# Kernel tuning notes

Hardware: AMD Instinct MI355X
Metric: run time of the kernel (lower is better)

Reference implementation:

```python
import jax, jax.numpy as jnp
import numpy as np

B, S, H = 32, 2048, 1024
A = 1024  # attention_hidden_size
EPS = 1e-5


def setup_inputs() -> dict:
    key = jax.random.key(0)
    ks = jax.random.split(key, 16)
    sc_h = 1.0 / np.sqrt(H)
    sc_a = 1.0 / np.sqrt(A)
    sc_2h = 1.0 / np.sqrt(2 * H)
    return {
        "seq_states": jax.random.normal(ks[0], (B, S, H), jnp.float32),
        "q_state": jax.random.normal(ks[1], (B, H), jnp.float32),
        "Wk": jax.random.uniform(ks[2], (H, A), jnp.float32, -sc_h, sc_h),
        "bk": jax.random.uniform(ks[3], (A,), jnp.float32, -sc_h, sc_h),
        "Wq": jax.random.uniform(ks[4], (H, A), jnp.float32, -sc_h, sc_h),
        "bq": jax.random.uniform(ks[5], (A,), jnp.float32, -sc_h, sc_h),
        "Wg": jax.random.uniform(ks[6], (A, A), jnp.float32, -sc_a, sc_a),
        "bg": jax.random.uniform(ks[7], (A,), jnp.float32, -sc_a, sc_a),
        "Ws": jax.random.uniform(ks[8], (A, 1), jnp.float32, -sc_a, sc_a),
        "bs": jax.random.uniform(ks[9], (1,), jnp.float32, -sc_a, sc_a),
        "Wo": jax.random.uniform(ks[10], (2 * H, H), jnp.float32, -sc_2h, sc_2h),
        "bo": jax.random.uniform(ks[11], (H,), jnp.float32, -sc_2h, sc_2h),
        "gamma": jnp.ones((H,), jnp.float32),
        "beta": jnp.zeros((H,), jnp.float32),
    }


def reference(seq_states, q_state, Wk, bk, Wq, bq, Wg, bg, Ws, bs, Wo, bo, gamma, beta):
    keys = jnp.einsum("bsh,ha->bsa", seq_states, Wk) + bk          # [B,S,A]
    query = (q_state @ Wq + bq)[:, None, :]                          # [B,1,A]
    alignment = jnp.tanh(keys + query)                               # [B,S,A]
    gate = jax.nn.sigmoid(jnp.einsum("bsa,ac->bsc", alignment, Wg) + bg)
    gated = alignment * gate                                         # dropout p=0.0 -> identity
    scores = jnp.einsum("bsa,ao->bso", gated, Ws)[..., 0] + bs[0]    # [B,S]
    weights = jax.nn.softmax(scores, axis=1)                         # [B,S]
    context = jnp.einsum("bs,bsh->bh", weights, seq_states)          # [B,H]
    fused_in = jnp.concatenate([context, q_state], axis=-1)          # [B,2H]
    pre = fused_in @ Wo + bo + q_state                               # residual
    mu = jnp.mean(pre, axis=-1, keepdims=True)
    var = jnp.var(pre, axis=-1, keepdims=True)
    fused = (pre - mu) * jax.lax.rsqrt(var + EPS) * gamma + beta
    return (fused, weights)
```

## Files before the change

### kernel.cpp

```cpp
#include <hip/hip_runtime.h>

typedef __attribute__((ext_vector_type(8))) short bf16x8;
typedef __attribute__((ext_vector_type(8))) unsigned short ushort8;
typedef __attribute__((ext_vector_type(4))) unsigned short ushortx4;
typedef __attribute__((ext_vector_type(4))) float f32x4;

#define BM 256
#define BN 256
#define BK 64

__device__ __forceinline__ unsigned short f2bf(float f) {
  union { float f; unsigned u; } c; c.f = f;
  return (unsigned short)((c.u + 0x7fffu + ((c.u >> 16) & 1u)) >> 16);
}
__device__ __forceinline__ float bf2f(unsigned short u) {
  union { unsigned u; float f; } c; c.u = ((unsigned)u) << 16;
  return c.f;
}
__device__ __forceinline__ float fast_tanh(float x) {
  float e = __expf(2.f * x);
  return 1.f - 2.f * __builtin_amdgcn_rcpf(e + 1.f);
}
__device__ __forceinline__ float fast_sigmoid(float x) {
  return __builtin_amdgcn_rcpf(1.f + __expf(-x));
}
__device__ __forceinline__ void gload16(const void* g, void* lds) {
  __builtin_amdgcn_global_load_lds(
      (const __attribute__((address_space(1))) unsigned int*)g,
      (__attribute__((address_space(3))) unsigned int*)lds, 16, 0, 0);
}
__device__ __forceinline__ void bar() {
  asm volatile("" ::: "memory");
  __builtin_amdgcn_s_barrier();
  asm volatile("" ::: "memory");
}
__device__ __forceinline__ void lgkm0_fence() {
  asm volatile("s_waitcnt lgkmcnt(0)" ::: "memory");
  __builtin_amdgcn_sched_barrier(0);
}
template <int N> __device__ __forceinline__ void vwait() {
  if constexpr (N < 0) {
  } else if constexpr (N == 6) asm volatile("s_waitcnt vmcnt(6)" ::: "memory");
  else if constexpr (N == 0) asm volatile("s_waitcnt vmcnt(0)" ::: "memory");
}

__device__ __forceinline__ void mfma_q(const bf16x8 (&av)[2][4], const bf16x8 (&bv)[2][2],
                                       int qm, int qn, f32x4 (&acc)[8][4]) {
  __builtin_amdgcn_s_setprio(1);
#pragma unroll
  for (int kk = 0; kk < 2; ++kk)
#pragma unroll
    for (int i = 0; i < 4; ++i)
#pragma unroll
      for (int j = 0; j < 2; ++j)
        acc[qm * 4 + i][qn * 2 + j] = __builtin_amdgcn_mfma_f32_16x16x32_bf16(
            av[kk][i], bv[kk][j], acc[qm * 4 + i][qn * 2 + j], 0, 0, 0);
  __builtin_amdgcn_s_setprio(0);
}

template <bool S1, bool S234, int WEND>
__device__ __forceinline__ void ktile(
    const char* rA0, const char* rA1,
    const char* rB0, const char* rB1,
    char* dNxtA, char* dCurA, char* dCurB,
    const unsigned short* pA0, const unsigned short* pA1,
    const unsigned short* pB0, const unsigned short* pB1,
    int kA1, int k2, f32x4 (&acc)[8][4]) {
  bf16x8 av[2][4], a2[2][4], bv0[2][2], bv1[2][2];
#pragma unroll
  for (int kk = 0; kk < 2; ++kk) {
    const char* ra = kk ? rA1 : rA0;
    const char* rb = kk ? rB1 : rB0;
#pragma unroll
    for (int i = 0; i < 4; ++i) av[kk][i] = *(const bf16x8*)(ra + i * 2048);
#pragma unroll
    for (int j = 0; j < 2; ++j) bv0[kk][j] = *(const bf16x8*)(rb + j * 2048);
  }
  if (S1) {
    gload16(pA0 + 65536 + kA1, dNxtA + 16384);
    gload16(pA1 + 65536 + kA1, dNxtA + 16384 + 8192);
  }
  bar();
  lgkm0_fence();
  mfma_q(av, bv0, 0, 0, acc);
  bar();
#pragma unroll
  for (int kk = 0; kk < 2; ++kk) {
    const char* rb = kk ? rB1 : rB0;
#pragma unroll
    for (int j = 0; j < 2; ++j) bv1[kk][j] = *(const bf16x8*)(rb + 16384 + j * 2048);
  }
  if (S234) {
    gload16(pA0 + k2, dCurA);
    gload16(pA1 + k2, dCurA + 8192);
  }
  bar();
  lgkm0_fence();
  mfma_q(av, bv1, 0, 1, acc);
  bar();
#pragma unroll
  for (int kk = 0; kk < 2; ++kk) {
    const char* ra = kk ? rA1 : rA0;
#pragma unroll
    for (int i = 0; i < 4; ++i) a2[kk][i] = *(const bf16x8*)(ra + 16384 + i * 2048);
  }
  if (S234) {
    gload16(pB0 + k2, dCurB);
    gload16(pB1 + k2, dCurB + 8192);
  }
  bar();
  lgkm0_fence();
  mfma_q(a2, bv1, 1, 1, acc);
  bar();
  if (S234) {
    gload16(pB0 + 32768 + k2, dCurB + 16384);
    gload16(pB1 + 32768 + k2, dCurB + 16384 + 8192);
  }
  bar();
  mfma_q(a2, bv0, 1, 0, acc);
  vwait<WEND>();
  bar();
}

#define GEMM_SETUP_AND_PIPELINE(Ag, Bg)                                                    \
  int t = threadIdx.x, lane = t & 63, wave = t >> 6;                                       \
  int wr = wave >> 2, wc = wave & 3;                                                       \
  int sl0 = ((lane >> 4) ^ (lane & 7)) * 16;                                               \
  int sl1 = (((lane >> 4) + 4) ^ (lane & 7)) * 16;                                         \
  int aLane = (wr * 64 + (lane & 15)) * 128;                                               \
  int bLane = (wc * 32 + (lane & 15)) * 128;                                               \
  const char* rA0k0 = (const char*)As0 + aLane + sl0;                                      \
  const char* rA0k1 = (const char*)As0 + aLane + sl1;                                      \
  const char* rA1k0 = (const char*)As1 + aLane + sl0;                                      \
  const char* rA1k1 = (const char*)As1 + aLane + sl1;                                      \
  const char* rB0k0 = (const char*)Bs0 + bLane + sl0;                                      \
  const char* rB0k1 = (const char*)Bs0 + bLane + sl1;                                      \
  const char* rB1k0 = (const char*)Bs1 + bLane + sl0;                                      \
  const char* rB1k1 = (const char*)Bs1 + bLane + sl1;                                      \
  char* dA0 = (char*)As0 + t * 16;                                                         \
  char* dA1 = (char*)As1 + t * 16;                                                         \
  char* dB0 = (char*)Bs0 + t * 16;                                                         \
  char* dB1 = (char*)Bs1 + t * 16;                                                         \
  int l3 = t >> 3;                                                                         \
  int sgE = ((t & 7) ^ (l3 & 7)) * 8;                                                      \
  const unsigned short* pA0 = Ag + (size_t)(m0 + l3) * 1024 + sgE;                         \
  const unsigned short* pA1 = pA0 + (size_t)128 * 1024;                                    \
  int nB0 = ((l3 >> 5) << 6) + (l3 & 31);                                                  \
  const unsigned short* pB0 = Bg + (size_t)(n0 + nB0) * 1024 + sgE;                        \
  const unsigned short* pB1 = pB0 + (size_t)128 * 1024;                                    \
  f32x4 acc[8][4] = {};                                                                    \
                      \
  gload16(pA0, dA0); gload16(pA1, dA0 + 8192);                                             \
  gload16(pB0, dB0); gload16(pB1, dB0 + 8192);                                             \
  gload16(pB0 + 32768, dB0 + 16384); gload16(pB1 + 32768, dB0 + 16384 + 8192);             \
  gload16(pA0 + 65536, dA0 + 16384); gload16(pA1 + 65536, dA0 + 16384 + 8192);             \
  gload16(pA0 + 64, dA1); gload16(pA1 + 64, dA1 + 8192);                                   \
  gload16(pB0 + 64, dB1); gload16(pB1 + 64, dB1 + 8192);                                   \
  gload16(pB0 + 32768 + 64, dB1 + 16384); gload16(pB1 + 32768 + 64, dB1 + 16384 + 8192);   \
  vwait<6>();                                                                              \
  bar();                                                                                   \
  _Pragma("unroll 1") for (int kt = 0; kt < 14; kt += 2) {                                 \
    ktile<true, true, 6>(rA0k0, rA0k1, rB0k0, rB0k1, dA1, dA0, dB0, pA0, pA1, pB0, pB1,    \
                         (kt + 1) * 64, (kt + 2) * 64, acc);                               \
    ktile<true, true, 6>(rA1k0, rA1k1, rB1k0, rB1k1, dA0, dA1, dB1, pA0, pA1, pB0, pB1,    \
                         (kt + 2) * 64, (kt + 3) * 64, acc);                               \
  }                                                                                        \
  ktile<true, false, 0>(rA0k0, rA0k1, rB0k0, rB0k1, dA1, dA0, dB0, pA0, pA1, pB0, pB1,     \
                        15 * 64, 0, acc);                                                  \
  ktile<false, false, -1>(rA1k0, rA1k1, rB1k0, rB1k1, dA0, dA1, dB1, pA0, pA1, pB0, pB1,   \
                          0, 0, acc);

__device__ __forceinline__ void tile_coords(int bid, int& m0, int& n0, int& nt) {
  int lin = (bid & 7) * 128 + (bid >> 3);
  int mt = lin >> 2;
  nt = lin & 3;
  m0 = mt * BM;
  n0 = nt * BN;
}

__global__ __launch_bounds__(256) void prep_kernel(
    const float* __restrict__ seq, unsigned short* __restrict__ seqb,
    const float* __restrict__ Wk, const float* __restrict__ Wg,
    unsigned short* __restrict__ WkT, unsigned short* __restrict__ WgT,
    const float* __restrict__ q, const float* __restrict__ Wq,
    float* __restrict__ qp) {
  __shared__ float smem[4160];
  int bid = blockIdx.x, t = threadIdx.x;
  if (bid < 2048) {
    size_t i = ((size_t)bid * 256 + t) * 8;
    const size_t stride = (size_t)2048 * 256 * 8;
    for (; i < (size_t)67108864; i += stride) {
      f32x4 v0 = *(const f32x4*)(seq + i);
      f32x4 v1 = *(const f32x4*)(seq + i + 4);
      ushort8 o;
#pragma unroll
      for (int k = 0; k < 4; ++k) { o[k] = f2bf(v0[k]); o[k + 4] = f2bf(v1[k]); }
      *(ushort8*)(seqb + i) = o;
    }
  } else if (bid < 2560) {
    int b2 = bid - 2048;
    int mat = b2 >> 8;
    int tid = b2 & 255;
    int tr = tid >> 4, tc = tid & 15;
    const float* src = mat ? Wg : Wk;
    unsigned short* dst = mat ? WgT : WkT;
    int r0 = tr * 64, c0 = tc * 64;
    int lr = t >> 6, lc = t & 63;
#pragma unroll
    for (int i = 0; i < 16; ++i) {
      int r = i * 4 + lr;
      smem[r * 65 + lc] = src[(size_t)(r0 + r) * 1024 + c0 + lc];
    }
    __syncthreads();
#pragma unroll
    for (int i = 0; i < 16; ++i) {
      int r = i * 4 + lr;
      dst[(size_t)(c0 + r) * 1024 + r0 + lc] = f2bf(smem[lc * 65 + r]);
    }
  } else {
    int b3 = bid - 2560;
    int ac = b3 & 3, hc = b3 >> 2;
    int h0 = hc * 128;
    for (int i = t; i < 4096; i += 256) {
      int b = i >> 7, hh = i & 127;
      smem[b * 128 + hh] = q[(size_t)b * 1024 + h0 + hh];
    }
    __syncthreads();
    int a = ac * 256 + t;
    float acc[32] = {};
    for (int hh = 0; hh < 128; hh += 4) {
      float w0 = Wq[(size_t)(h0 + hh) * 1024 + a];
      float w1 = Wq[(size_t)(h0 + hh + 1) * 1024 + a];
      float w2 = Wq[(size_t)(h0 + hh + 2) * 1024 + a];
      float w3 = Wq[(size_t)(h0 + hh + 3) * 1024 + a];
#pragma unroll
      for (int b = 0; b < 32; ++b) {
        f32x4 qv = *(const f32x4*)&smem[b * 128 + hh];
        acc[b] += qv[0] * w0 + qv[1] * w1 + qv[2] * w2 + qv[3] * w3;
      }
    }
#pragma unroll
    for (int b = 0; b < 32; ++b) qp[((size_t)(hc * 32 + b)) * 1024 + a] = acc[b];
  }
}

__global__ __launch_bounds__(512, 2) void gemm1_kernel(
    const unsigned short* __restrict__ seqb, const unsigned short* __restrict__ WkT,
    const float* __restrict__ qp, const float* __restrict__ bq,
    const float* __restrict__ bk, unsigned short* __restrict__ alignb) {
  __shared__ unsigned short As0[BM * BK], Bs0[BN * BK], As1[BM * BK], Bs1[BN * BK];
  int m0, n0, nt;
  tile_coords(blockIdx.x, m0, n0, nt);
  GEMM_SETUP_AND_PIPELINE(seqb, WkT)

  int bidx = m0 >> 11;
  float qv[4];
#pragma unroll
  for (int ni = 0; ni < 4; ++ni) {
    int col = n0 + wc * 64 + ni * 16 + (lane & 15);
    float s = bq[col] + bk[col];
#pragma unroll
    for (int hc = 0; hc < 8; ++hc) s += qp[((size_t)(hc * 32 + bidx)) * 1024 + col];
    qv[ni] = s;
  }
#pragma unroll
  for (int mi = 0; mi < 8; ++mi) {
    int row0 = m0 + wr * 128 + mi * 16 + ((lane >> 4) * 4);
#pragma unroll
    for (int ni = 0; ni < 4; ++ni) {
      int col = n0 + wc * 64 + ni * 16 + (lane & 15);
#pragma unroll
      for (int j = 0; j < 4; ++j) {
        float v = fast_tanh(acc[mi][ni][j] + qv[ni]);
        alignb[(size_t)(row0 + j) * 1024 + col] = f2bf(v);
      }
    }
  }
}

__global__ __launch_bounds__(512, 2) void gemm2_kernel(
    const unsigned short* __restrict__ alignb, const unsigned short* __restrict__ WgT,
    const float* __restrict__ bg, const float* __restrict__ Ws,
    float* __restrict__ scores_part) {
  __shared__ unsigned short As0[BM * BK], Bs0[BN * BK], As1[BM * BK], Bs1[BN * BK];
  __shared__ float sred[BM * 4];
  int m0, n0, nt;
  tile_coords(blockIdx.x, m0, n0, nt);
  GEMM_SETUP_AND_PIPELINE(alignb, WgT)

#pragma unroll
  for (int mi = 0; mi < 8; ++mi) {
#pragma unroll
    for (int j = 0; j < 4; ++j) {
      int rloc = wr * 128 + mi * 16 + ((lane >> 4) * 4) + j;
      int row = m0 + rloc;
      float p = 0.f;
#pragma unroll
      for (int ni = 0; ni < 4; ++ni) {
        int col = n0 + wc * 64 + ni * 16 + (lane & 15);
        float gate = fast_sigmoid(acc[mi][ni][j] + bg[col]);
        float al = bf2f(alignb[(size_t)row * 1024 + col]);
        p += al * gate * Ws[col];
      }
      p += __shfl_xor(p, 1);
      p += __shfl_xor(p, 2);
      p += __shfl_xor(p, 4);
      p += __shfl_xor(p, 8);
      if ((lane & 15) == 0) sred[rloc * 4 + wc] = p;
    }
  }
  __syncthreads();
  if (t < 256)
    scores_part[(size_t)nt * 65536 + m0 + t] =
        sred[t * 4] + sred[t * 4 + 1] + sred[t * 4 + 2] + sred[t * 4 + 3];
}

__global__ __launch_bounds__(256) void softmax_kernel(const float* __restrict__ sp,
                                                      float* __restrict__ wout) {
  __shared__ float red[256];
  int b = blockIdx.x, t = threadIdx.x;
  float sc[8];
  float lmax = -1e30f;
#pragma unroll
  for (int i = 0; i < 8; ++i) {
    int s = i * 256 + t;
    float v = 0.f;
#pragma unroll
    for (int n = 0; n < 4; ++n) v += sp[(size_t)n * 65536 + b * 2048 + s];
    sc[i] = v;
    lmax = fmaxf(lmax, v);
  }
  red[t] = lmax;
  __syncthreads();
  for (int off = 128; off > 0; off >>= 1) {
    if (t < off) red[t] = fmaxf(red[t], red[t + off]);
    __syncthreads();
  }
  float mx = red[0];
  __syncthreads();
  float lsum = 0.f;
#pragma unroll
  for (int i = 0; i < 8; ++i) {
    sc[i] = expf(sc[i] - mx);
    lsum += sc[i];
  }
  red[t] = lsum;
  __syncthreads();
  for (int off = 128; off > 0; off >>= 1) {
    if (t < off) red[t] += red[t + off];
    __syncthreads();
  }
  float inv = 1.f / red[0];
#pragma unroll
  for (int i = 0; i < 8; ++i) wout[(size_t)b * 2048 + i * 256 + t] = sc[i] * inv;
}

__global__ __launch_bounds__(256) void context_kernel(const unsigned short* __restrict__ seqb,
                                                      const float* __restrict__ wts,
                                                      float* __restrict__ ctx_part) {
  __shared__ float wsh[256];
  int b = blockIdx.x, t = threadIdx.x, s0 = blockIdx.z * 256;
  int h0 = t * 4;
  wsh[t] = wts[(size_t)b * 2048 + s0 + t];
  __syncthreads();
  float a0 = 0.f, a1 = 0.f, a2 = 0.f, a3 = 0.f;
  const unsigned short* p = seqb + ((size_t)b * 2048 + s0) * 1024 + h0;
#pragma unroll 4
  for (int s = 0; s < 256; ++s) {
    ushortx4 v = *(const ushortx4*)(p + (size_t)s * 1024);
    float w = wsh[s];
    a0 += w * bf2f(v[0]);
    a1 += w * bf2f(v[1]);
    a2 += w * bf2f(v[2]);
    a3 += w * bf2f(v[3]);
  }
  float* dst = ctx_part + (size_t)(blockIdx.z * 32 + b) * 1024 + h0;
  dst[0] = a0; dst[1] = a1; dst[2] = a2; dst[3] = a3;
}

__global__ __launch_bounds__(256) void pre_kernel(const float* __restrict__ ctx_part,
                                                  const float* __restrict__ q,
                                                  const float* __restrict__ Wo,
                                                  float* __restrict__ pre_part) {
  __shared__ float fin[32 * 128];
  int kc = blockIdx.x, hc = blockIdx.y, t = threadIdx.x;
  int k0 = kc * 128, h0 = hc * 256;
  for (int i = t; i < 4096; i += 256) {
    int b = i >> 7, kk = i & 127, k = k0 + kk;
    float f;
    if (k < 1024) {
      f = 0.f;
#pragma unroll
      for (int s = 0; s < 8; ++s) f += ctx_part[((size_t)(s * 32 + b)) * 1024 + k];
    } else {
      f = q[(size_t)b * 1024 + (k - 1024)];
    }
    fin[b * 128 + kk] = f;
  }
  __syncthreads();
  int h = h0 + t;
  float acc[32] = {};
  for (int kk = 0; kk < 128; kk += 4) {
    float w0 = Wo[(size_t)(k0 + kk) * 1024 + h];
    float w1 = Wo[(size_t)(k0 + kk + 1) * 1024 + h];
    float w2 = Wo[(size_t)(k0 + kk + 2) * 1024 + h];
    float w3 = Wo[(size_t)(k0 + kk + 3) * 1024 + h];
#pragma unroll
    for (int b = 0; b < 32; ++b) {
      f32x4 fv = *(const f32x4*)&fin[b * 128 + kk];
      acc[b] += fv[0] * w0 + fv[1] * w1 + fv[2] * w2 + fv[3] * w3;
    }
  }
#pragma unroll
  for (int b = 0; b < 32; ++b) pre_part[((size_t)(kc * 32 + b)) * 1024 + h] = acc[b];
}

__global__ __launch_bounds__(256) void ln_kernel(const float* __restrict__ pre_part,
                                                 const float* __restrict__ q,
                                                 const float* __restrict__ bo,
                                                 const float* __restrict__ gamma,
                                                 const float* __restrict__ beta,
                                                 float* __restrict__ outF) {
  __shared__ float red[256];
  int b = blockIdx.x, t = threadIdx.x;
  float v[4];
  float lsum = 0.f;
#pragma unroll
  for (int i = 0; i < 4; ++i) {
    int h = i * 256 + t;
    float x = bo[h] + q[(size_t)b * 1024 + h];
#pragma unroll
    for (int kc = 0; kc < 16; ++kc) x += pre_part[((size_t)(kc * 32 + b)) * 1024 + h];
    v[i] = x;
    lsum += x;
  }
  red[t] = lsum;
  __syncthreads();
  for (int off = 128; off > 0; off >>= 1) {
    if (t < off) red[t] += red[t + off];
    __syncthreads();
  }
  float mu = red[0] * (1.f / 1024.f);
  __syncthreads();
  float lv = 0.f;
#pragma unroll
  for (int i = 0; i < 4; ++i) {
    float d = v[i] - mu;
    lv += d * d;
  }
  red[t] = lv;
  __syncthreads();
  for (int off = 128; off > 0; off >>= 1) {
    if (t < off) red[t] += red[t + off];
    __syncthreads();
  }
  float var = red[0] * (1.f / 1024.f);
  float rs = rsqrtf(var + 1e-5f);
#pragma unroll
  for (int i = 0; i < 4; ++i) {
    int h = i * 256 + t;
    outF[(size_t)b * 1024 + h] = (v[i] - mu) * rs * gamma[h] + beta[h];
  }
}

extern "C" void kernel_launch(void* const* d_in, const int* in_sizes, int n_in,
                              void* d_out, int out_size, void* d_ws, size_t ws_size,
                              hipStream_t stream) {
  const float* seq = (const float*)d_in[0];
  const float* q = (const float*)d_in[1];
  const float* Wk = (const float*)d_in[2];
  const float* bk = (const float*)d_in[3];
  const float* Wq = (const float*)d_in[4];
  const float* bq = (const float*)d_in[5];
  const float* Wg = (const float*)d_in[6];
  const float* bg = (const float*)d_in[7];
  const float* Ws = (const float*)d_in[8];
  const float* Wo = (const float*)d_in[10];
  const float* bo = (const float*)d_in[11];
  const float* gamma = (const float*)d_in[12];
  const float* beta = (const float*)d_in[13];

  float* outF = (float*)d_out;
  float* outW = outF + 32 * 1024;

  char* ws = (char*)d_ws;
  unsigned short* alignb = (unsigned short*)ws;  ws += (size_t)134217728;
  unsigned short* seqb = (unsigned short*)ws;    ws += (size_t)134217728;
  unsigned short* WkT = (unsigned short*)ws;     ws += 2097152;
  unsigned short* WgT = (unsigned short*)ws;     ws += 2097152;
  float* qp = (float*)ws;                        ws += 1048576;
  float* scores_part = (float*)ws;               ws += 1048576;
  float* ctx_part = (float*)ws;                  ws += 1048576;
  float* pre_part = (float*)ws;                  ws += 2097152;
  if (ws_size < (size_t)(ws - (char*)d_ws)) return;

  prep_kernel<<<2592, 256, 0, stream>>>(seq, seqb, Wk, Wg, WkT, WgT, q, Wq, qp);
  gemm1_kernel<<<1024, 512, 0, stream>>>(seqb, WkT, qp, bq, bk, alignb);
  gemm2_kernel<<<1024, 512, 0, stream>>>(alignb, WgT, bg, Ws, scores_part);
  softmax_kernel<<<32, 256, 0, stream>>>(scores_part, outW);
  context_kernel<<<dim3(32, 1, 8), 256, 0, stream>>>(seqb, outW, ctx_part);
  pre_kernel<<<dim3(16, 4), 256, 0, stream>>>(ctx_part, q, Wo, pre_part);
  ln_kernel<<<32, 256, 0, stream>>>(pre_part, q, bo, gamma, beta, outF);
}
```

Baseline: 501.8 us.

## Restructure GEMM k-tile pipeline to per-k-half MFMA blocks and split context wider

The GEMM inner k-tile is reorganised. Each phase now runs a full 4x4 MFMA block over one k-half (two phases per A row-half) instead of quadrant-by-quadrant across both k-halves. The prefetch schedule now loads only one tile ahead, with vmcnt(2) waits, rather than keeping two tiles in flight. This cuts register pressure and changes how global loads into LDS overlap with MFMA, at the risk of exposing more load latency. Separately, the context reduction is split into 16 sequence chunks instead of 8 for more parallelism, which adds more partial sums for pre_kernel to reduce.

```diff
diff --git a/kernel.cpp b/kernel.cpp
--- a/kernel.cpp
+++ b/kernel.cpp
@@ -40,85 +40,78 @@
 }
 template <int N> __device__ __forceinline__ void vwait() {
   if constexpr (N < 0) {
-  } else if constexpr (N == 6) asm volatile("s_waitcnt vmcnt(6)" ::: "memory");
+  } else if constexpr (N == 2) asm volatile("s_waitcnt vmcnt(2)" ::: "memory");
   else if constexpr (N == 0) asm volatile("s_waitcnt vmcnt(0)" ::: "memory");
 }
 
-__device__ __forceinline__ void mfma_q(const bf16x8 (&av)[2][4], const bf16x8 (&bv)[2][2],
-                                       int qm, int qn, f32x4 (&acc)[8][4]) {
+__device__ __forceinline__ void mfma16(const bf16x8 (&a)[4], const bf16x8 (&b)[4], int ro,
+                                       f32x4 (&acc)[8][4]) {
   __builtin_amdgcn_s_setprio(1);
 #pragma unroll
-  for (int kk = 0; kk < 2; ++kk)
-#pragma unroll
-    for (int i = 0; i < 4; ++i)
-#pragma unroll
-      for (int j = 0; j < 2; ++j)
-        acc[qm * 4 + i][qn * 2 + j] = __builtin_amdgcn_mfma_f32_16x16x32_bf16(
-            av[kk][i], bv[kk][j], acc[qm * 4 + i][qn * 2 + j], 0, 0, 0);
+  for (int i = 0; i < 4; ++i)
+#pragma unroll
+    for (int n = 0; n < 4; ++n)
+      acc[ro + i][n] =
+          __builtin_amdgcn_mfma_f32_16x16x32_bf16(a[i], b[n], acc[ro + i][n], 0, 0, 0);
   __builtin_amdgcn_s_setprio(0);
 }
 
-template <bool S1, bool S234, int WEND>
+template <bool ST, int W1, int W4>
 __device__ __forceinline__ void ktile(
-    const char* rA0, const char* rA1,
-    const char* rB0, const char* rB1,
-    char* dNxtA, char* dCurA, char* dCurB,
+    const char* rAk0, const char* rAk1,
+    const char* rBk0, const char* rBk1,
+    char* dNA, char* dNB,
     const unsigned short* pA0, const unsigned short* pA1,
     const unsigned short* pB0, const unsigned short* pB1,
-    int kA1, int k2, f32x4 (&acc)[8][4]) {
-  bf16x8 av[2][4], a2[2][4], bv0[2][2], bv1[2][2];
-#pragma unroll
-  for (int kk = 0; kk < 2; ++kk) {
-    const char* ra = kk ? rA1 : rA0;
-    const char* rb = kk ? rB1 : rB0;
-#pragma unroll
-    for (int i = 0; i < 4; ++i) av[kk][i] = *(const bf16x8*)(ra + i * 2048);
-#pragma unroll
-    for (int j = 0; j < 2; ++j) bv0[kk][j] = *(const bf16x8*)(rb + j * 2048);
-  }
-  if (S1) {
-    gload16(pA0 + 65536 + kA1, dNxtA + 16384);
-    gload16(pA1 + 65536 + kA1, dNxtA + 16384 + 8192);
-  }
+    int kN, f32x4 (&acc)[8][4]) {
+  bf16x8 a[4], a2[4], b[4];
+#pragma unroll
+  for (int i = 0; i < 4; ++i) a[i] = *(const bf16x8*)(rAk0 + i * 2048);
+#pragma unroll
+  for (int n = 0; n < 4; ++n)
+    b[n] = *(const bf16x8*)(rBk0 + (n >> 1) * 16384 + (n & 1) * 2048);
+  if (ST) {
+    gload16(pB0 + 32768 + kN, dNB + 16384);
+    gload16(pB1 + 32768 + kN, dNB + 16384 + 8192);
+  }
+  vwait<W1>();
   bar();
   lgkm0_fence();
-  mfma_q(av, bv0, 0, 0, acc);
-  bar();
-#pragma unroll
-  for (int kk = 0; kk < 2; ++kk) {
-    const char* rb = kk ? rB1 : rB0;
-#pragma unroll
-    for (int j = 0; j < 2; ++j) bv1[kk][j] = *(const bf16x8*)(rb + 16384 + j * 2048);
-  }
-  if (S234) {
-    gload16(pA0 + k2, dCurA);
-    gload16(pA1 + k2, dCurA + 8192);
+  mfma16(a, b, 0, acc);
+  bar();
+#pragma unroll
+  for (int i = 0; i < 4; ++i) a2[i] = *(const bf16x8*)(rAk0 + 16384 + i * 2048);
+  if (ST) {
+    gload16(pA0 + kN, dNA);
+    gload16(pA1 + kN, dNA + 8192);
   }
   bar();
   lgkm0_fence();
-  mfma_q(av, bv1, 0, 1, acc);
-  bar();
-#pragma unroll
-  for (int kk = 0; kk < 2; ++kk) {
-    const char* ra = kk ? rA1 : rA0;
-#pragma unroll
-    for (int i = 0; i < 4; ++i) a2[kk][i] = *(const bf16x8*)(ra + 16384 + i * 2048);
-  }
-  if (S234) {
-    gload16(pB0 + k2, dCurB);
-    gload16(pB1 + k2, dCurB + 8192);
+  mfma16(a2, b, 4, acc);
+  bar();
+#pragma unroll
+  for (int i = 0; i < 4; ++i) a[i] = *(const bf16x8*)(rAk1 + i * 2048);
+#pragma unroll
+  for (int n = 0; n < 4; ++n)
+    b[n] = *(const bf16x8*)(rBk1 + (n >> 1) * 16384 + (n & 1) * 2048);
+  if (ST) {
+    gload16(pB0 + kN, dNB);
+    gload16(pB1 + kN, dNB + 8192);
   }
   bar();
   lgkm0_fence();
-  mfma_q(a2, bv1, 1, 1, acc);
-  bar();
-  if (S234) {
-    gload16(pB0 + 32768 + k2, dCurB + 16384);
-    gload16(pB1 + 32768 + k2, dCurB + 16384 + 8192);
-  }
-  bar();
-  mfma_q(a2, bv0, 1, 0, acc);
-  vwait<WEND>();
+  mfma16(a, b, 0, acc);
+  bar();
+#pragma unroll
+  for (int i = 0; i < 4; ++i) a2[i] = *(const bf16x8*)(rAk1 + 16384 + i * 2048);
+  if (ST) {
+    gload16(pA0 + 65536 + kN, dNA + 16384);
+    gload16(pA1 + 65536 + kN, dNA + 16384 + 8192);
+  }
+  vwait<W4>();
+  bar();
+  lgkm0_fence();
+  mfma16(a2, b, 4, acc);
   bar();
 }
 
@@ -149,26 +142,21 @@
   const unsigned short* pB0 = Bg + (size_t)(n0 + nB0) * 1024 + sgE;                        \
   const unsigned short* pB1 = pB0 + (size_t)128 * 1024;                                    \
   f32x4 acc[8][4] = {};                                                                    \
-                      \
+             \
   gload16(pA0, dA0); gload16(pA1, dA0 + 8192);                                             \
   gload16(pB0, dB0); gload16(pB1, dB0 + 8192);                                             \
   gload16(pB0 + 32768, dB0 + 16384); gload16(pB1 + 32768, dB0 + 16384 + 8192);             \
   gload16(pA0 + 65536, dA0 + 16384); gload16(pA1 + 65536, dA0 + 16384 + 8192);             \
-  gload16(pA0 + 64, dA1); gload16(pA1 + 64, dA1 + 8192);                                   \
-  gload16(pB0 + 64, dB1); gload16(pB1 + 64, dB1 + 8192);                                   \
-  gload16(pB0 + 32768 + 64, dB1 + 16384); gload16(pB1 + 32768 + 64, dB1 + 16384 + 8192);   \
-  vwait<6>();                                                                              \
+  vwait<2>();                                                                              \
   bar();                                                                                   \
   _Pragma("unroll 1") for (int kt = 0; kt < 14; kt += 2) {                                 \
-    ktile<true, true, 6>(rA0k0, rA0k1, rB0k0, rB0k1, dA1, dA0, dB0, pA0, pA1, pB0, pB1,    \
-                         (kt + 1) * 64, (kt + 2) * 64, acc);                               \
-    ktile<true, true, 6>(rA1k0, rA1k1, rB1k0, rB1k1, dA0, dA1, dB1, pA0, pA1, pB0, pB1,    \
-                         (kt + 2) * 64, (kt + 3) * 64, acc);                               \
+    ktile<true, 2, 2>(rA0k0, rA0k1, rB0k0, rB0k1, dA1, dB1, pA0, pA1, pB0, pB1,            \
+                      (kt + 1) * 64, acc);                                                 \
+    ktile<true, 2, 2>(rA1k0, rA1k1, rB1k0, rB1k1, dA0, dB0, pA0, pA1, pB0, pB1,            \
+                      (kt + 2) * 64, acc);                                                 \
   }                                                                                        \
-  ktile<true, false, 0>(rA0k0, rA0k1, rB0k0, rB0k1, dA1, dA0, dB0, pA0, pA1, pB0, pB1,     \
-                        15 * 64, 0, acc);                                                  \
-  ktile<false, false, -1>(rA1k0, rA1k1, rB1k0, rB1k1, dA0, dA1, dB1, pA0, pA1, pB0, pB1,   \
-                          0, 0, acc);
+  ktile<true, 2, 2>(rA0k0, rA0k1, rB0k0, rB0k1, dA1, dB1, pA0, pA1, pB0, pB1, 960, acc);   \
+  ktile<false, 0, -1>(rA1k0, rA1k1, rB1k0, rB1k1, dA0, dB0, pA0, pA1, pB0, pB1, 0, acc);
 
 __device__ __forceinline__ void tile_coords(int bid, int& m0, int& n0, int& nt) {
   int lin = (bid & 7) * 128 + (bid >> 3);
@@ -358,15 +346,15 @@
 __global__ __launch_bounds__(256) void context_kernel(const unsigned short* __restrict__ seqb,
                                                       const float* __restrict__ wts,
                                                       float* __restrict__ ctx_part) {
-  __shared__ float wsh[256];
-  int b = blockIdx.x, t = threadIdx.x, s0 = blockIdx.z * 256;
+  __shared__ float wsh[128];
+  int b = blockIdx.x, t = threadIdx.x, s0 = blockIdx.z * 128;
   int h0 = t * 4;
-  wsh[t] = wts[(size_t)b * 2048 + s0 + t];
+  if (t < 128) wsh[t] = wts[(size_t)b * 2048 + s0 + t];
   __syncthreads();
   float a0 = 0.f, a1 = 0.f, a2 = 0.f, a3 = 0.f;
   const unsigned short* p = seqb + ((size_t)b * 2048 + s0) * 1024 + h0;
 #pragma unroll 4
-  for (int s = 0; s < 256; ++s) {
+  for (int s = 0; s < 128; ++s) {
     ushortx4 v = *(const ushortx4*)(p + (size_t)s * 1024);
     float w = wsh[s];
     a0 += w * bf2f(v[0]);
@@ -391,7 +379,7 @@
     if (k < 1024) {
       f = 0.f;
 #pragma unroll
-      for (int s = 0; s < 8; ++s) f += ctx_part[((size_t)(s * 32 + b)) * 1024 + k];
+      for (int s = 0; s < 16; ++s) f += ctx_part[((size_t)(s * 32 + b)) * 1024 + k];
     } else {
       f = q[(size_t)b * 1024 + (k - 1024)];
     }
@@ -490,7 +478,7 @@
   unsigned short* WgT = (unsigned short*)ws;     ws += 2097152;
   float* qp = (float*)ws;                        ws += 1048576;
   float* scores_part = (float*)ws;               ws += 1048576;
-  float* ctx_part = (float*)ws;                  ws += 1048576;
+  float* ctx_part = (float*)ws;                  ws += 2097152;
   float* pre_part = (float*)ws;                  ws += 2097152;
   if (ws_size < (size_t)(ws - (char*)d_ws)) return;
 
@@ -498,7 +486,7 @@
   gemm1_kernel<<<1024, 512, 0, stream>>>(seqb, WkT, qp, bq, bk, alignb);
   gemm2_kernel<<<1024, 512, 0, stream>>>(alignb, WgT, bg, Ws, scores_part);
   softmax_kernel<<<32, 256, 0, stream>>>(scores_part, outW);
-  context_kernel<<<dim3(32, 1, 8), 256, 0, stream>>>(seqb, outW, ctx_part);
+  context_kernel<<<dim3(32, 1, 16), 256, 0, stream>>>(seqb, outW, ctx_part);
   pre_kernel<<<dim3(16, 4), 256, 0, stream>>>(ctx_part, q, Wo, pre_part);
   ln_kernel<<<32, 256, 0, stream>>>(pre_part, q, bo, gamma, beta, outF);
 }
```

Result: no change. 509.5 us (+1.5%).
